# Kernel optimization log

Measured on AMD Instinct MI355X. Metric: run time of the kernel, lower is better.

The kernel has to match this reference:

```python
import jax, jax.numpy as jnp
import numpy as np

FP8_MAX = 448.0
EPS = 1e-12


def setup_inputs() -> dict:
    key = jax.random.key(0)
    k1, k2 = jax.random.split(key)
    x = jax.random.normal(k1, (4, 2048, 4096), dtype=jnp.float32)
    # kaiming-uniform-like init scale for weight
    weight = jax.random.normal(k2, (4096, 4096), dtype=jnp.float32) * 0.02
    bias = jnp.zeros((4096,), dtype=jnp.float32)
    return {"x": x, "weight": weight, "bias": bias}


def reference(x, weight, bias):
    # per-tensor fake-quant of activations
    input_scale = jnp.maximum(jnp.max(jnp.abs(x)) / FP8_MAX, EPS)
    x_q = jnp.round(jnp.clip(x / input_scale, -FP8_MAX, FP8_MAX))
    # per-tensor fake-quant of weight
    weight_scale = jnp.maximum(jnp.max(jnp.abs(weight)) / FP8_MAX, EPS)
    weight_q = jnp.round(jnp.clip(weight / weight_scale, -FP8_MAX, FP8_MAX))
    # GEMM in quantized domain, then dequant rescale + bias
    out_q = jnp.einsum('bsi,oi->bso', x_q, weight_q)  # [B,S,out]
    out = (out_q * (input_scale * weight_scale)).astype(x.dtype) + bias
    return out
```

## Files before the change

### kernel.cpp

```cpp
#include <hip/hip_runtime.h>

#define FP8_MAX 448.0f
#define EPSF 1e-12f

#define BM 256
#define BN 256
#define BK 64

typedef __attribute__((ext_vector_type(8))) _Float16 half8;
typedef __attribute__((ext_vector_type(4))) float floatx4;

#define VMCNT(n) asm volatile("s_waitcnt vmcnt(" #n ")" ::: "memory")

__device__ inline void async_copy16(const void* gp, void* lp) {
  __builtin_amdgcn_global_load_lds(
      (const __attribute__((address_space(1))) unsigned int*)gp,
      (__attribute__((address_space(3))) unsigned int*)lp,
      16, 0, 0);
}

__global__ void absmax_kernel(const float* __restrict__ in, int n4,
                              unsigned* __restrict__ out) {
  int tid = blockIdx.x * blockDim.x + threadIdx.x;
  int stride = gridDim.x * blockDim.x;
  const float4* in4 = (const float4*)in;
  float m = 0.f;
  for (int i = tid; i < n4; i += stride) {
    float4 v = in4[i];
    m = fmaxf(m, fmaxf(fmaxf(fabsf(v.x), fabsf(v.y)),
                       fmaxf(fabsf(v.z), fabsf(v.w))));
  }
  for (int off = 32; off > 0; off >>= 1)
    m = fmaxf(m, __shfl_down(m, off, 64));
  __shared__ float smax[4];
  int lane = threadIdx.x & 63, w = threadIdx.x >> 6;
  if (lane == 0) smax[w] = m;
  __syncthreads();
  if (threadIdx.x == 0) {
    float b = fmaxf(fmaxf(smax[0], smax[1]), fmaxf(smax[2], smax[3]));
    atomicMax(out, __float_as_uint(b));
  }
}

__global__ void quant_kernel(const float* __restrict__ in,
                             _Float16* __restrict__ out, int n8,
                             const unsigned* __restrict__ amax_bits) {
  const float scale = fmaxf(__uint_as_float(*amax_bits) / FP8_MAX, EPSF);
  int tid = blockIdx.x * blockDim.x + threadIdx.x;
  int stride = gridDim.x * blockDim.x;
  const float4* in4 = (const float4*)in;
  half8* out8 = (half8*)out;
  for (int i = tid; i < n8; i += stride) {
    float4 a = in4[2 * i], b = in4[2 * i + 1];
    half8 h;
    h[0] = (_Float16)rintf(fminf(fmaxf(a.x / scale, -FP8_MAX), FP8_MAX));
    h[1] = (_Float16)rintf(fminf(fmaxf(a.y / scale, -FP8_MAX), FP8_MAX));
    h[2] = (_Float16)rintf(fminf(fmaxf(a.z / scale, -FP8_MAX), FP8_MAX));
    h[3] = (_Float16)rintf(fminf(fmaxf(a.w / scale, -FP8_MAX), FP8_MAX));
    h[4] = (_Float16)rintf(fminf(fmaxf(b.x / scale, -FP8_MAX), FP8_MAX));
    h[5] = (_Float16)rintf(fminf(fmaxf(b.y / scale, -FP8_MAX), FP8_MAX));
    h[6] = (_Float16)rintf(fminf(fmaxf(b.z / scale, -FP8_MAX), FP8_MAX));
    h[7] = (_Float16)rintf(fminf(fmaxf(b.w / scale, -FP8_MAX), FP8_MAX));
    out8[i] = h;
  }
}

__global__ __launch_bounds__(512, 2) void gemm8_kernel(
    const _Float16* __restrict__ A,
    const _Float16* __restrict__ B,
    const float* __restrict__ bias, const unsigned* __restrict__ amax,
    float* __restrict__ C,
    int M, int N, int K) {
  __shared__ __align__(16) _Float16 As[2][BM * BK];
  __shared__ __align__(16) _Float16 Bs[2][BN * BK];

  const int tid = threadIdx.x;
  const int w = tid >> 6;
  const int lane = tid & 63;
  const int wr = w >> 2;
  const int wc = w & 3;

  const int nwg = gridDim.x;
  const int cpx = nwg >> 3;
  const int swz = (blockIdx.x & 7) * cpx + (blockIdx.x >> 3);
  const int nbn = N / BN;
  const int bm = swz / nbn;
  const int bn = swz % nbn;

  const _Float16* Ab = A + (size_t)bm * BM * K;
  const _Float16* Bb = B + (size_t)bn * BN * K;

  const int srow8 = w * 8 + (lane >> 3);
  const int gd8 = ((lane & 7) ^ ((lane >> 3) & 7)) * 8;
  const _Float16* Ag = Ab + (size_t)srow8 * K + gd8;
  const _Float16* Bg = Bb + (size_t)srow8 * K + gd8;

  auto stageA = [&](int kt, int h) {
#pragma unroll
    for (int r = 2 * h; r < 2 * h + 2; ++r)
      async_copy16(Ag + (size_t)(r * 64) * K + kt * BK,
                   (void*)&As[kt & 1][(r * 64 + w * 8) * BK]);
  };
  auto stageB = [&](int kt, int h) {
#pragma unroll
    for (int r = 2 * h; r < 2 * h + 2; ++r)
      async_copy16(Bg + (size_t)(r * 64) * K + kt * BK,
                   (void*)&Bs[kt & 1][(r * 64 + w * 8) * BK]);
  };

  const int lr = lane & 15;
  const int hi = lane >> 4;
  const int aoff = (wr * 128 + lr) * BK;
  const int boff = (wc * 64 + lr) * BK;
  const int g0 = (hi ^ (lr & 7)) * 8;
  const int g1 = ((4 + hi) ^ (lr & 7)) * 8;

  half8 aL[4][2], aH[4][2], bL[2][2], bH[2][2];
  floatx4 acc[8][4] = {};
  const int nt = K / BK;

  stageA(0, 0); stageA(0, 1); stageB(0, 0); stageB(0, 1);
  stageA(1, 0); stageA(1, 1);
  VMCNT(4);
  __builtin_amdgcn_s_barrier();

  for (int t = 0; t < nt; ++t) {
    const int b = t & 1;
    const _Float16* Asb = &As[b][0];
    const _Float16* Bsb = &Bs[b][0];

#pragma unroll
    for (int m = 0; m < 4; ++m) {
      aL[m][0] = *(const half8*)&Asb[aoff + m * 16 * BK + g0];
      aL[m][1] = *(const half8*)&Asb[aoff + m * 16 * BK + g1];
    }
#pragma unroll
    for (int n = 0; n < 2; ++n) {
      bL[n][0] = *(const half8*)&Bsb[boff + n * 16 * BK + g0];
      bL[n][1] = *(const half8*)&Bsb[boff + n * 16 * BK + g1];
    }
    if (t + 1 < nt) stageB(t + 1, 0);
    __builtin_amdgcn_s_barrier();
    asm volatile("s_waitcnt lgkmcnt(0)" ::: "memory");
    __builtin_amdgcn_s_setprio(1);
#pragma unroll
    for (int m = 0; m < 4; ++m)
#pragma unroll
      for (int n = 0; n < 2; ++n)
#pragma unroll
        for (int kk = 0; kk < 2; ++kk)
          acc[m][n] = __builtin_amdgcn_mfma_f32_16x16x32_f16(
              aL[m][kk], bL[n][kk], acc[m][n], 0, 0, 0);
    __builtin_amdgcn_s_setprio(0);
    __builtin_amdgcn_s_barrier();

#pragma unroll
    for (int m = 0; m < 4; ++m) {
      aH[m][0] = *(const half8*)&Asb[aoff + (64 + m * 16) * BK + g0];
      aH[m][1] = *(const half8*)&Asb[aoff + (64 + m * 16) * BK + g1];
    }
#pragma unroll
    for (int n = 0; n < 2; ++n) {
      bH[n][0] = *(const half8*)&Bsb[boff + (32 + n * 16) * BK + g0];
      bH[n][1] = *(const half8*)&Bsb[boff + (32 + n * 16) * BK + g1];
    }
    if (t + 1 < nt) stageB(t + 1, 1);
    __builtin_amdgcn_s_barrier();
    asm volatile("s_waitcnt lgkmcnt(0)" ::: "memory");
    __builtin_amdgcn_s_setprio(1);
#pragma unroll
    for (int m = 0; m < 4; ++m)
#pragma unroll
      for (int n = 0; n < 2; ++n)
#pragma unroll
        for (int kk = 0; kk < 2; ++kk)
          acc[m][2 + n] = __builtin_amdgcn_mfma_f32_16x16x32_f16(
              aL[m][kk], bH[n][kk], acc[m][2 + n], 0, 0, 0);
    __builtin_amdgcn_s_setprio(0);
    __builtin_amdgcn_s_barrier();

    if (t + 2 < nt) stageA(t + 2, 0);
    __builtin_amdgcn_s_setprio(1);
#pragma unroll
    for (int m = 0; m < 4; ++m)
#pragma unroll
      for (int n = 0; n < 2; ++n)
#pragma unroll
        for (int kk = 0; kk < 2; ++kk)
          acc[4 + m][n] = __builtin_amdgcn_mfma_f32_16x16x32_f16(
              aH[m][kk], bL[n][kk], acc[4 + m][n], 0, 0, 0);
    __builtin_amdgcn_s_setprio(0);
    __builtin_amdgcn_s_barrier();

    if (t + 2 < nt) stageA(t + 2, 1);
    __builtin_amdgcn_s_setprio(1);
#pragma unroll
    for (int m = 0; m < 4; ++m)
#pragma unroll
      for (int n = 0; n < 2; ++n)
#pragma unroll
        for (int kk = 0; kk < 2; ++kk)
          acc[4 + m][2 + n] = __builtin_amdgcn_mfma_f32_16x16x32_f16(
              aH[m][kk], bH[n][kk], acc[4 + m][2 + n], 0, 0, 0);
    __builtin_amdgcn_s_setprio(0);
    if (t + 2 < nt) {
      VMCNT(4);
    } else {
      VMCNT(0);
    }
    __builtin_amdgcn_s_barrier();
  }

  const float sx = fmaxf(__uint_as_float(amax[0]) / FP8_MAX, EPSF);
  const float sw = fmaxf(__uint_as_float(amax[1]) / FP8_MAX, EPSF);
  const float s = sx * sw;

  const int row0 = bm * BM + wr * 128 + hi * 4;
  const int col0 = bn * BN + wc * 64 + lr;
  float bv[4];
#pragma unroll
  for (int n = 0; n < 4; ++n) bv[n] = bias[col0 + n * 16];

#pragma unroll
  for (int m = 0; m < 8; ++m) {
#pragma unroll
    for (int n = 0; n < 4; ++n) {
      const size_t base = (size_t)(row0 + m * 16) * N + col0 + n * 16;
#pragma unroll
      for (int r = 0; r < 4; ++r)
        C[base + (size_t)r * N] = acc[m][n][r] * s + bv[n];
    }
  }
}

extern "C" void kernel_launch(void* const* d_in, const int* in_sizes, int n_in,
                              void* d_out, int out_size, void* d_ws,
                              size_t ws_size, hipStream_t stream) {
  const float* x = (const float*)d_in[0];
  const float* wgt = (const float*)d_in[1];
  const float* bias = (const float*)d_in[2];
  float* out = (float*)d_out;

  const int N = in_sizes[2];
  const int K = in_sizes[1] / N;
  const int M = in_sizes[0] / K;

  unsigned* amax = (unsigned*)d_ws;
  _Float16* xq = (_Float16*)((char*)d_ws + 256);
  _Float16* wq =
      (_Float16*)((char*)d_ws + 256 + (size_t)M * K * sizeof(_Float16));

  hipMemsetAsync(d_ws, 0, 8, stream);
  absmax_kernel<<<2048, 256, 0, stream>>>(x, M * K / 4, amax);
  absmax_kernel<<<1024, 256, 0, stream>>>(wgt, N * K / 4, amax + 1);
  quant_kernel<<<2048, 256, 0, stream>>>(x, xq, M * K / 8, amax);
  quant_kernel<<<1024, 256, 0, stream>>>(wgt, wq, N * K / 8, amax + 1);

  gemm8_kernel<<<dim3((M / BM) * (N / BN)), 512, 0, stream>>>(
      xq, wq, bias, amax, out, M, N, K);
}
```

Before: 395.6 us.

## Unroll GEMM main loop by two and split tile into L/H halves for finer staging

Unrolls the K loop by two with explicit buffer 0/1 addressing, and remaps each wave's sub-tile so the low and high halves of A and B come from separate 128-row regions of the LDS tile. Global-to-LDS staging is reissued at finer granularity: each half of the next tile is loaded as soon as its LDS region is no longer needed, and vmcnt/lgkmcnt waits are adjusted. The goal is more overlap of global loads with MFMA work and fewer stalls on the prefetch wait. The trade-off is more barriers, a larger unrolled body, and tight correctness reliance on the waitcnt accounting.

```diff
diff --git a/kernel.cpp b/kernel.cpp
--- a/kernel.cpp
+++ b/kernel.cpp
@@ -11,6 +11,7 @@
 typedef __attribute__((ext_vector_type(4))) float floatx4;
 
 #define VMCNT(n) asm volatile("s_waitcnt vmcnt(" #n ")" ::: "memory")
+#define LGKM(n) asm volatile("s_waitcnt lgkmcnt(" #n ")" ::: "memory")
 
 __device__ inline void async_copy16(const void* gp, void* lp) {
   __builtin_amdgcn_global_load_lds(
@@ -110,38 +111,42 @@
 
   const int lr = lane & 15;
   const int hi = lane >> 4;
-  const int aoff = (wr * 128 + lr) * BK;
-  const int boff = (wc * 64 + lr) * BK;
   const int g0 = (hi ^ (lr & 7)) * 8;
   const int g1 = ((4 + hi) ^ (lr & 7)) * 8;
+  const int aoffL = (wr * 64 + lr) * BK;
+  const int aoffH = (128 + wr * 64 + lr) * BK;
+  const int boffL = (wc * 32 + lr) * BK;
+  const int boffH = (128 + wc * 32 + lr) * BK;
 
   half8 aL[4][2], aH[4][2], bL[2][2], bH[2][2];
   floatx4 acc[8][4] = {};
   const int nt = K / BK;
 
-  stageA(0, 0); stageA(0, 1); stageB(0, 0); stageB(0, 1);
-  stageA(1, 0); stageA(1, 1);
-  VMCNT(4);
+  stageA(0, 0); stageB(0, 0); stageB(0, 1); stageA(0, 1);
+  stageA(1, 0); stageB(1, 0); stageB(1, 1);
+  VMCNT(6);
   __builtin_amdgcn_s_barrier();
 
-  for (int t = 0; t < nt; ++t) {
-    const int b = t & 1;
-    const _Float16* Asb = &As[b][0];
-    const _Float16* Bsb = &Bs[b][0];
+  for (int t = 0; t < nt; t += 2) {
+    const _Float16* As0 = &As[0][0];
+    const _Float16* Bs0 = &Bs[0][0];
+    const _Float16* As1 = &As[1][0];
+    const _Float16* Bs1 = &Bs[1][0];
 
 #pragma unroll
     for (int m = 0; m < 4; ++m) {
-      aL[m][0] = *(const half8*)&Asb[aoff + m * 16 * BK + g0];
-      aL[m][1] = *(const half8*)&Asb[aoff + m * 16 * BK + g1];
+      aL[m][0] = *(const half8*)&As0[aoffL + m * 16 * BK + g0];
+      aL[m][1] = *(const half8*)&As0[aoffL + m * 16 * BK + g1];
     }
 #pragma unroll
     for (int n = 0; n < 2; ++n) {
-      bL[n][0] = *(const half8*)&Bsb[boff + n * 16 * BK + g0];
-      bL[n][1] = *(const half8*)&Bsb[boff + n * 16 * BK + g1];
-    }
-    if (t + 1 < nt) stageB(t + 1, 0);
-    __builtin_amdgcn_s_barrier();
-    asm volatile("s_waitcnt lgkmcnt(0)" ::: "memory");
+      bL[n][0] = *(const half8*)&Bs0[boffL + n * 16 * BK + g0];
+      bL[n][1] = *(const half8*)&Bs0[boffL + n * 16 * BK + g1];
+    }
+    stageA(t + 1, 1);
+    LGKM(8);
+    __builtin_amdgcn_s_barrier();
+    LGKM(0);
     __builtin_amdgcn_s_setprio(1);
 #pragma unroll
     for (int m = 0; m < 4; ++m)
@@ -155,18 +160,13 @@
     __builtin_amdgcn_s_barrier();
 
 #pragma unroll
-    for (int m = 0; m < 4; ++m) {
-      aH[m][0] = *(const half8*)&Asb[aoff + (64 + m * 16) * BK + g0];
-      aH[m][1] = *(const half8*)&Asb[aoff + (64 + m * 16) * BK + g1];
-    }
-#pragma unroll
     for (int n = 0; n < 2; ++n) {
-      bH[n][0] = *(const half8*)&Bsb[boff + (32 + n * 16) * BK + g0];
-      bH[n][1] = *(const half8*)&Bsb[boff + (32 + n * 16) * BK + g1];
-    }
-    if (t + 1 < nt) stageB(t + 1, 1);
-    __builtin_amdgcn_s_barrier();
-    asm volatile("s_waitcnt lgkmcnt(0)" ::: "memory");
+      bH[n][0] = *(const half8*)&Bs0[boffH + n * 16 * BK + g0];
+      bH[n][1] = *(const half8*)&Bs0[boffH + n * 16 * BK + g1];
+    }
+    if (t + 2 < nt) stageA(t + 2, 0);
+    __builtin_amdgcn_s_barrier();
+    LGKM(0);
     __builtin_amdgcn_s_setprio(1);
 #pragma unroll
     for (int m = 0; m < 4; ++m)
@@ -179,7 +179,14 @@
     __builtin_amdgcn_s_setprio(0);
     __builtin_amdgcn_s_barrier();
 
-    if (t + 2 < nt) stageA(t + 2, 0);
+#pragma unroll
+    for (int m = 0; m < 4; ++m) {
+      aH[m][0] = *(const half8*)&As0[aoffH + m * 16 * BK + g0];
+      aH[m][1] = *(const half8*)&As0[aoffH + m * 16 * BK + g1];
+    }
+    if (t + 2 < nt) stageB(t + 2, 0);
+    __builtin_amdgcn_s_barrier();
+    LGKM(0);
     __builtin_amdgcn_s_setprio(1);
 #pragma unroll
     for (int m = 0; m < 4; ++m)
@@ -192,7 +199,8 @@
     __builtin_amdgcn_s_setprio(0);
     __builtin_amdgcn_s_barrier();
 
-    if (t + 2 < nt) stageA(t + 2, 1);
+    if (t + 2 < nt) stageB(t + 2, 1);
+    __builtin_amdgcn_s_barrier();
     __builtin_amdgcn_s_setprio(1);
 #pragma unroll
     for (int m = 0; m < 4; ++m)
@@ -203,11 +211,88 @@
           acc[4 + m][2 + n] = __builtin_amdgcn_mfma_f32_16x16x32_f16(
               aH[m][kk], bH[n][kk], acc[4 + m][2 + n], 0, 0, 0);
     __builtin_amdgcn_s_setprio(0);
-    if (t + 2 < nt) {
-      VMCNT(4);
-    } else {
-      VMCNT(0);
-    }
+    if (t + 2 < nt) { VMCNT(6); } else { VMCNT(0); }
+    __builtin_amdgcn_s_barrier();
+
+#pragma unroll
+    for (int m = 0; m < 4; ++m) {
+      aL[m][0] = *(const half8*)&As1[aoffL + m * 16 * BK + g0];
+      aL[m][1] = *(const half8*)&As1[aoffL + m * 16 * BK + g1];
+    }
+#pragma unroll
+    for (int n = 0; n < 2; ++n) {
+      bL[n][0] = *(const half8*)&Bs1[boffL + n * 16 * BK + g0];
+      bL[n][1] = *(const half8*)&Bs1[boffL + n * 16 * BK + g1];
+    }
+    if (t + 2 < nt) stageA(t + 2, 1);
+    LGKM(8);
+    __builtin_amdgcn_s_barrier();
+    LGKM(0);
+    __builtin_amdgcn_s_setprio(1);
+#pragma unroll
+    for (int m = 0; m < 4; ++m)
+#pragma unroll
+      for (int n = 0; n < 2; ++n)
+#pragma unroll
+        for (int kk = 0; kk < 2; ++kk)
+          acc[m][n] = __builtin_amdgcn_mfma_f32_16x16x32_f16(
+              aL[m][kk], bL[n][kk], acc[m][n], 0, 0, 0);
+    __builtin_amdgcn_s_setprio(0);
+    __builtin_amdgcn_s_barrier();
+
+#pragma unroll
+    for (int n = 0; n < 2; ++n) {
+      bH[n][0] = *(const half8*)&Bs1[boffH + n * 16 * BK + g0];
+      bH[n][1] = *(const half8*)&Bs1[boffH + n * 16 * BK + g1];
+    }
+    if (t + 3 < nt) stageA(t + 3, 0);
+    __builtin_amdgcn_s_barrier();
+    LGKM(0);
+    __builtin_amdgcn_s_setprio(1);
+#pragma unroll
+    for (int m = 0; m < 4; ++m)
+#pragma unroll
+      for (int n = 0; n < 2; ++n)
+#pragma unroll
+        for (int kk = 0; kk < 2; ++kk)
+          acc[m][2 + n] = __builtin_amdgcn_mfma_f32_16x16x32_f16(
+              aL[m][kk], bH[n][kk], acc[m][2 + n], 0, 0, 0);
+    __builtin_amdgcn_s_setprio(0);
+    __builtin_amdgcn_s_barrier();
+
+#pragma unroll
+    for (int m = 0; m < 4; ++m) {
+      aH[m][0] = *(const half8*)&As1[aoffH + m * 16 * BK + g0];
+      aH[m][1] = *(const half8*)&As1[aoffH + m * 16 * BK + g1];
+    }
+    if (t + 3 < nt) stageB(t + 3, 0);
+    __builtin_amdgcn_s_barrier();
+    LGKM(0);
+    __builtin_amdgcn_s_setprio(1);
+#pragma unroll
+    for (int m = 0; m < 4; ++m)
+#pragma unroll
+      for (int n = 0; n < 2; ++n)
+#pragma unroll
+        for (int kk = 0; kk < 2; ++kk)
+          acc[4 + m][n] = __builtin_amdgcn_mfma_f32_16x16x32_f16(
+              aH[m][kk], bL[n][kk], acc[4 + m][n], 0, 0, 0);
+    __builtin_amdgcn_s_setprio(0);
+    __builtin_amdgcn_s_barrier();
+
+    if (t + 3 < nt) stageB(t + 3, 1);
+    __builtin_amdgcn_s_barrier();
+    __builtin_amdgcn_s_setprio(1);
+#pragma unroll
+    for (int m = 0; m < 4; ++m)
+#pragma unroll
+      for (int n = 0; n < 2; ++n)
+#pragma unroll
+        for (int kk = 0; kk < 2; ++kk)
+          acc[4 + m][2 + n] = __builtin_amdgcn_mfma_f32_16x16x32_f16(
+              aH[m][kk], bH[n][kk], acc[4 + m][2 + n], 0, 0, 0);
+    __builtin_amdgcn_s_setprio(0);
+    if (t + 3 < nt) { VMCNT(6); } else { VMCNT(0); }
     __builtin_amdgcn_s_barrier();
   }
 
@@ -215,17 +300,18 @@
   const float sw = fmaxf(__uint_as_float(amax[1]) / FP8_MAX, EPSF);
   const float s = sx * sw;
 
-  const int row0 = bm * BM + wr * 128 + hi * 4;
-  const int col0 = bn * BN + wc * 64 + lr;
   float bv[4];
 #pragma unroll
-  for (int n = 0; n < 4; ++n) bv[n] = bias[col0 + n * 16];
+  for (int n = 0; n < 4; ++n)
+    bv[n] = bias[bn * BN + (n >> 1) * 128 + wc * 32 + (n & 1) * 16 + lr];
 
 #pragma unroll
   for (int m = 0; m < 8; ++m) {
 #pragma unroll
     for (int n = 0; n < 4; ++n) {
-      const size_t base = (size_t)(row0 + m * 16) * N + col0 + n * 16;
+      const int row = bm * BM + (m >> 2) * 128 + wr * 64 + (m & 3) * 16 + hi * 4;
+      const int col = bn * BN + (n >> 1) * 128 + wc * 32 + (n & 1) * 16 + lr;
+      const size_t base = (size_t)row * N + col;
 #pragma unroll
       for (int r = 0; r < 4; ++r)
         C[base + (size_t)r * N] = acc[m][n][r] * s + bv[n];
```

Measured after the change: 408.2 us. +3.2%, slower.
